# Kernel tuning notes

Hardware: AMD Instinct MI355X
Metric: run time of the kernel (lower is better)

## Reference

```python
import jax, jax.numpy as jnp
import numpy as np
from jax import lax

B, C_IN, C_OUT, K, N_W, L = 32, 256, 256, 7, 8, 4096
SQ = C_IN // 32  # squeezed dim = 8
STRIDE, PAD = 1, 3


def setup_inputs() -> dict:
    key = jax.random.key(0)
    ks = jax.random.split(key, 8)
    s = 0.05
    return {
        "x": jax.random.normal(ks[0], (B, C_IN, L), dtype=jnp.float32),
        "conv_weight": jax.random.normal(ks[1], (C_OUT, C_IN, K, N_W), dtype=jnp.float32) * s,
        "w1": jax.random.normal(ks[2], (C_IN, SQ), dtype=jnp.float32) * s,   # linear1 weight (x @ w1)
        "b1": jax.random.normal(ks[3], (SQ,), dtype=jnp.float32) * s,
        "wk": jax.random.normal(ks[4], (SQ, K), dtype=jnp.float32) * s,      # kernel head
        "wi": jax.random.normal(ks[5], (SQ, C_IN), dtype=jnp.float32) * s,   # inc head
        "wo": jax.random.normal(ks[6], (SQ, C_OUT), dtype=jnp.float32) * s,  # outc head
        "wn": jax.random.normal(ks[7], (SQ, N_W), dtype=jnp.float32) * s,    # nums head
    }


def reference(x, conv_weight, w1, b1, wk, wi, wo, wn):
    # SqueezeFeedForward: AdaptiveAvgPool1d(1) == mean over length, then Linear + exact GELU
    pooled = jnp.mean(x, axis=-1)                        # [B, C_in]
    h = jax.nn.gelu(pooled @ w1 + b1, approximate=False)  # [B, SQ]

    kr = jax.nn.sigmoid(h @ wk)          # [B, K]
    inc = jax.nn.sigmoid(h @ wi)         # [B, C_in]
    outc = jax.nn.sigmoid(h @ wo)        # [B, C_out]
    nums = jax.nn.softmax(h @ wn, -1)    # [B, N_w]

    # Per-sample mixed weights: sum over num_weight of 4-way outer-product gated base weight
    w = jnp.einsum('bk,bi,bo,bn,oikn->boik', kr, inc, outc, nums, conv_weight)  # [B,O,I,K]

    b, o, i, k = w.shape
    l = x.shape[-1]
    # Batched per-sample conv via grouped conv: groups = B
    lhs = x.reshape(1, b * i, l)         # [1, B*I, L]
    rhs = w.reshape(b * o, i, k)         # [B*O, I, K]
    out = lax.conv_general_dilated(
        lhs, rhs,
        window_strides=(STRIDE,),
        padding=[(PAD, PAD)],
        dimension_numbers=('NCH', 'OIH', 'NCH'),
        feature_group_count=b,
    )
    return out.reshape(b, o, -1)         # [B, O, L_out]
```

## Files before the change

### kernel.cpp

```cpp
#include <hip/hip_runtime.h>
#include <hip/hip_bf16.h>
#include <math.h>

#define B_   32
#define CI   256
#define CO   256
#define KW   7
#define NW   8
#define SQD  8
#define L_   4096

typedef __attribute__((ext_vector_type(8))) __bf16 bf16x8;
typedef __attribute__((ext_vector_type(4))) float  f32x4;

static __device__ __forceinline__ unsigned short f2bf(float f) {
    unsigned int u = __builtin_bit_cast(unsigned int, f);
    u += 0x7FFFu + ((u >> 16) & 1u);
    return (unsigned short)(u >> 16);
}

__global__ __launch_bounds__(256) void k1_mean(
        const float* __restrict__ x, float* __restrict__ pooled) {
    int row = blockIdx.x;
    const float* p = x + (size_t)row * L_;
    int t = threadIdx.x;
    float s = 0.f;
#pragma unroll
    for (int it = 0; it < 4; ++it) {
        float4 v = *(const float4*)(p + (size_t)(t + 256 * it) * 4);
        s += v.x + v.y + v.z + v.w;
    }
    for (int m = 1; m <= 32; m <<= 1) s += __shfl_xor(s, m);
    __shared__ float wsum[4];
    if ((t & 63) == 0) wsum[t >> 6] = s;
    __syncthreads();
    if (t == 0)
        pooled[row] = (wsum[0] + wsum[1] + wsum[2] + wsum[3]) * (1.0f / L_);
}

__global__ __launch_bounds__(64) void k2_gates(
        const float* __restrict__ pooled,
        const float* __restrict__ w1, const float* __restrict__ b1,
        const float* __restrict__ wk, const float* __restrict__ wi,
        const float* __restrict__ wo, const float* __restrict__ wn,
        float* __restrict__ kr,
        float* __restrict__ inc,
        float* __restrict__ outc,
        float* __restrict__ nums)
{
    int b = blockIdx.x, lane = threadIdx.x;
    float pc[4];
#pragma unroll
    for (int j = 0; j < 4; ++j)
        pc[j] = pooled[b * CI + lane + 64 * j];
    float h[SQD];
#pragma unroll
    for (int s = 0; s < SQD; ++s) {
        float ps = 0.f;
#pragma unroll
        for (int j = 0; j < 4; ++j)
            ps += pc[j] * w1[(lane + 64 * j) * SQD + s];
        for (int m = 1; m <= 32; m <<= 1) ps += __shfl_xor(ps, m);
        float z = ps + b1[s];
        h[s] = 0.5f * z * (1.0f + erff(z * 0.70710678118654752f));
    }
    if (lane < KW) {
        float a = 0.f;
#pragma unroll
        for (int s = 0; s < SQD; ++s) a += h[s] * wk[s * KW + lane];
        kr[b * 8 + lane] = 1.0f / (1.0f + expf(-a));
    }
    if (lane < NW) {
        float e[NW]; float mx = -1e30f;
#pragma unroll
        for (int n = 0; n < NW; ++n) {
            float a = 0.f;
#pragma unroll
            for (int s = 0; s < SQD; ++s) a += h[s] * wn[s * NW + n];
            e[n] = a; mx = fmaxf(mx, a);
        }
        float den = 0.f;
#pragma unroll
        for (int n = 0; n < NW; ++n) den += expf(e[n] - mx);
        nums[b * NW + lane] = expf(e[lane] - mx) / den;
    }
#pragma unroll
    for (int j = 0; j < 4; ++j) {
        int c = lane + 64 * j;
        float a = 0.f, o2 = 0.f;
#pragma unroll
        for (int s = 0; s < SQD; ++s) {
            a  += h[s] * wi[s * CI + c];
            o2 += h[s] * wo[s * CO + c];
        }
        inc[b * CI + c]  = 1.0f / (1.0f + expf(-a));
        outc[b * CO + c] = 1.0f / (1.0f + expf(-o2));
    }
}

__global__ __launch_bounds__(256) void k3_wgen(
        const float* __restrict__ cw,
        const float* __restrict__ kr, const float* __restrict__ inc,
        const float* __restrict__ outc, const float* __restrict__ nums,
        unsigned short* __restrict__ W2) {
    __shared__ float s_nums[B_][NW];
    __shared__ float s_kr[B_][KW];
    __shared__ float s_inc[B_][32];
    __shared__ float s_outc[B_][8];
    int t = threadIdx.x;
    int ic = blockIdx.x & 7, o0 = (blockIdx.x >> 3) * 8;
    s_nums[t >> 3][t & 7] = nums[t];
    if (t < B_ * KW) s_kr[t / KW][t % KW] = kr[(t / KW) * 8 + (t % KW)];
    for (int u = t; u < 32 * 32; u += 256) {
        int bb = u >> 5, ii = u & 31;
        s_inc[bb][ii] = inc[bb * CI + ic * 32 + ii];
    }
    for (int u = t; u < 32 * 8; u += 256) {
        int bb = u >> 3, oo = u & 7;
        s_outc[bb][oo] = outc[bb * CO + o0 + oo];
    }
    __syncthreads();
    int ii = t & 31, oo = t >> 5;
    int o = o0 + oo, i = ic * 32 + ii;
    float cwv[KW][NW];
    const float* p = cw + ((size_t)(o * CI + i)) * (KW * NW);
#pragma unroll
    for (int k = 0; k < KW; ++k)
#pragma unroll
        for (int n = 0; n < NW; ++n) cwv[k][n] = p[k * NW + n];
    for (int bb = 0; bb < B_; ++bb) {
        float gio = s_inc[bb][ii] * s_outc[bb][oo];
#pragma unroll
        for (int k = 0; k < KW; ++k) {
            float sk = 0.f;
#pragma unroll
            for (int n = 0; n < NW; ++n) sk += s_nums[bb][n] * cwv[k][n];
            float w = s_kr[bb][k] * gio * sk;
            W2[(((size_t)(bb * KW + k) * 8 + ic) * CO + o) * 32 + ii] = f2bf(w);
        }
    }
}

__global__ __launch_bounds__(512, 4) void k4_conv(
        const float* __restrict__ x,
        const unsigned short* __restrict__ W2,
        float* __restrict__ out) {
    __shared__ __align__(16) unsigned short xs[134 * 256];
    int bid = blockIdx.x;
    int wg  = (bid & 7) * 128 + (bid >> 3);
    int b = wg >> 5, l0 = (wg & 31) * 128;
    int t = threadIdx.x;
    const float* xb = x + (size_t)b * CI * L_;

    {
        int c = t & 31;
        int i = t >> 5;
#pragma unroll 4
        for (int it = 0; it < 16; ++it, i += 16) {
            float4 v = *(const float4*)(xb + (size_t)i * L_ + l0 + c * 4);
            int u0 = i >> 3, isub = i & 7;
#pragma unroll
            for (int j = 0; j < 4; ++j) {
                int r = c * 4 + j + 3;
                xs[r * 256 + ((u0 ^ (r & 7)) * 8) + isub] = f2bf((&v.x)[j]);
            }
        }
    }
    for (int u = t; u < 6 * 256; u += 512) {
        int h = u >> 8, i = u & 255;
        int r = (h < 3) ? h : 128 + h;
        int gl = l0 - 3 + r;
        float f = (gl >= 0 && gl < L_) ? xb[(size_t)i * L_ + gl] : 0.f;
        xs[r * 256 + (((i >> 3) ^ (r & 7)) * 8) + (i & 7)] = f2bf(f);
    }
    __syncthreads();

    int lane = t & 63, wid = t >> 6;
    int o_base = wid * 32;
    int ml = lane & 15, kg = lane >> 4;

    f32x4 acc[2][8];
#pragma unroll
    for (int a = 0; a < 2; ++a)
#pragma unroll
        for (int c = 0; c < 8; ++c) acc[a][c] = (f32x4){0.f, 0.f, 0.f, 0.f};

    const unsigned short* wbase = W2 + (size_t)b * (KW * 8 * CO * 32);
    for (int k = 0; k < KW; ++k) {
        const unsigned short* wk_ = wbase + (size_t)k * (8 * CO * 32);
#pragma unroll
        for (int icc = 0; icc < 8; ++icc) {
            const unsigned short* wkc = wk_ + icc * (CO * 32);
            bf16x8 af[2];
#pragma unroll
            for (int mt = 0; mt < 2; ++mt)
                af[mt] = *(const bf16x8*)(wkc + (o_base + mt * 16 + ml) * 32 + kg * 8);
            bf16x8 bfr[8];
#pragma unroll
            for (int nt = 0; nt < 8; ++nt) {
                int r = nt * 16 + ml + k;
                int unit = (icc * 4 + kg) ^ (r & 7);
                bfr[nt] = *(const bf16x8*)(xs + r * 256 + unit * 8);
            }
            __builtin_amdgcn_s_setprio(1);
#pragma unroll
            for (int mt = 0; mt < 2; ++mt)
#pragma unroll
                for (int nt = 0; nt < 8; ++nt)
                    acc[mt][nt] = __builtin_amdgcn_mfma_f32_16x16x32_bf16(
                        af[mt], bfr[nt], acc[mt][nt], 0, 0, 0);
            __builtin_amdgcn_s_setprio(0);
        }
    }

#pragma unroll
    for (int mt = 0; mt < 2; ++mt) {
        int o = o_base + mt * 16 + kg * 4;
#pragma unroll
        for (int nt = 0; nt < 8; ++nt) {
            int l = l0 + nt * 16 + ml;
            float* po = out + ((size_t)(b * CO + o)) * L_ + l;
#pragma unroll
            for (int q = 0; q < 4; ++q)
                po[(size_t)q * L_] = acc[mt][nt][q];
        }
    }
}

extern "C" void kernel_launch(void* const* d_in, const int* in_sizes, int n_in,
                              void* d_out, int out_size, void* d_ws, size_t ws_size,
                              hipStream_t stream) {
    const float* x  = (const float*)d_in[0];
    const float* cw = (const float*)d_in[1];
    const float* w1 = (const float*)d_in[2];
    const float* b1 = (const float*)d_in[3];
    const float* wk = (const float*)d_in[4];
    const float* wi = (const float*)d_in[5];
    const float* wo = (const float*)d_in[6];
    const float* wn = (const float*)d_in[7];
    float* out = (float*)d_out;

    char* ws = (char*)d_ws;
    const size_t off_W2     = 0;
    const size_t off_pooled = 29360128;
    const size_t off_kr     = 29392896;
    const size_t off_inc    = 29393920;
    const size_t off_outc   = 29426688;
    const size_t off_nums   = 29459456;

    unsigned short* W2 = (unsigned short*)(ws + off_W2);
    float* pooled = (float*)(ws + off_pooled);
    float* kr     = (float*)(ws + off_kr);
    float* inc    = (float*)(ws + off_inc);
    float* outc   = (float*)(ws + off_outc);
    float* nums   = (float*)(ws + off_nums);

    k1_mean<<<B_ * CI, 256, 0, stream>>>(x, pooled);
    k2_gates<<<B_, 64, 0, stream>>>(pooled, w1, b1, wk, wi, wo, wn,
                                    kr, inc, outc, nums);
    k3_wgen<<<256, 256, 0, stream>>>(cw, kr, inc, outc, nums, W2);
    k4_conv<<<1024, 512, 0, stream>>>(x, W2, out);
}
```

Measured before the change: 175.4 us.

## Enlarge conv tile to 256 positions, 2D warp split, and double-buffer fragments

The conv kernel now processes 256 length positions per block instead of 128, with 8 waves split as 4 output-channel groups × 2 length halves, each wave computing a 64x128 output tile (4x8 MFMA tiles). The wider tile doubles reuse of the weight fragments loaded from global memory and of the staged input. The input staging packs four channels per 8-byte LDS store and uses a new XOR swizzle. The main loop software-pipelines fragment loads with two register buffers so loads for the next step overlap the current MFMAs. The cost is more registers and twice the LDS (occupancy hint lowered to 2) and half as many blocks.

```diff
diff --git a/kernel.cpp b/kernel.cpp
--- a/kernel.cpp
+++ b/kernel.cpp
@@ -18,6 +18,9 @@
     u += 0x7FFFu + ((u >> 16) & 1u);
     return (unsigned short)(u >> 16);
 }
+static __device__ __forceinline__ unsigned int pack2bf(float a, float b) {
+    return (unsigned int)f2bf(a) | ((unsigned int)f2bf(b) << 16);
+}
 
 __global__ __launch_bounds__(256) void k1_mean(
         const float* __restrict__ x, float* __restrict__ pooled) {
@@ -43,10 +46,8 @@
         const float* __restrict__ w1, const float* __restrict__ b1,
         const float* __restrict__ wk, const float* __restrict__ wi,
         const float* __restrict__ wo, const float* __restrict__ wn,
-        float* __restrict__ kr,
-        float* __restrict__ inc,
-        float* __restrict__ outc,
-        float* __restrict__ nums)
+        float* __restrict__ kr, float* __restrict__ inc,
+        float* __restrict__ outc, float* __restrict__ nums)
 {
     int b = blockIdx.x, lane = threadIdx.x;
     float pc[4];
@@ -141,84 +142,117 @@
     }
 }
 
-__global__ __launch_bounds__(512, 4) void k4_conv(
+__global__ __launch_bounds__(512, 2) void k4_conv(
         const float* __restrict__ x,
         const unsigned short* __restrict__ W2,
         float* __restrict__ out) {
-    __shared__ __align__(16) unsigned short xs[134 * 256];
+    __shared__ __align__(16) unsigned short xs[262 * 256];
     int bid = blockIdx.x;
-    int wg  = (bid & 7) * 128 + (bid >> 3);
-    int b = wg >> 5, l0 = (wg & 31) * 128;
+    int wg  = (bid & 7) * 64 + (bid >> 3);
+    int b = wg >> 4, l0 = (wg & 15) * 256;
     int t = threadIdx.x;
     const float* xb = x + (size_t)b * CI * L_;
 
     {
-        int c = t & 31;
-        int i = t >> 5;
-#pragma unroll 4
-        for (int it = 0; it < 16; ++it, i += 16) {
-            float4 v = *(const float4*)(xb + (size_t)i * L_ + l0 + c * 4);
-            int u0 = i >> 3, isub = i & 7;
+        int ch = (t & 31) + 32 * (t >> 8);
+        int g  = (t >> 5) & 7;
+#pragma unroll
+        for (int it = 0; it < 8; ++it) {
+            int i0 = g * 4 + it * 32;
+            float4 f0 = *(const float4*)(xb + (size_t)(i0 + 0) * L_ + l0 + ch * 4);
+            float4 f1 = *(const float4*)(xb + (size_t)(i0 + 1) * L_ + l0 + ch * 4);
+            float4 f2 = *(const float4*)(xb + (size_t)(i0 + 2) * L_ + l0 + ch * 4);
+            float4 f3 = *(const float4*)(xb + (size_t)(i0 + 3) * L_ + l0 + ch * 4);
+            int u = i0 >> 3, h = (i0 >> 2) & 1;
 #pragma unroll
             for (int j = 0; j < 4; ++j) {
-                int r = c * 4 + j + 3;
-                xs[r * 256 + ((u0 ^ (r & 7)) * 8) + isub] = f2bf((&v.x)[j]);
+                int r = 4 * ch + j + 3;
+                uint2 w;
+                w.x = pack2bf((&f0.x)[j], (&f1.x)[j]);
+                w.y = pack2bf((&f2.x)[j], (&f3.x)[j]);
+                int sw = (r & 7) ^ ((r >> 2) & 7);
+                *(uint2*)(xs + r * 256 + ((u ^ sw) * 8) + h * 4) = w;
             }
         }
     }
-    for (int u = t; u < 6 * 256; u += 512) {
-        int h = u >> 8, i = u & 255;
-        int r = (h < 3) ? h : 128 + h;
-        int gl = l0 - 3 + r;
-        float f = (gl >= 0 && gl < L_) ? xb[(size_t)i * L_ + gl] : 0.f;
-        xs[r * 256 + (((i >> 3) ^ (r & 7)) * 8) + (i & 7)] = f2bf(f);
+    if (t < 128) {
+        bool left = t < 64;
+        int tt = left ? t : t - 64;
+        int i0 = tt * 4;
+        int gl4 = left ? l0 - 4 : l0 + 256;
+        bool ok = left ? (l0 > 0) : (l0 + 256 < L_);
+        float4 f[4];
+#pragma unroll
+        for (int d = 0; d < 4; ++d)
+            f[d] = ok ? *(const float4*)(xb + (size_t)(i0 + d) * L_ + gl4)
+                      : make_float4(0.f, 0.f, 0.f, 0.f);
+        int u = i0 >> 3, h = (i0 >> 2) & 1;
+#pragma unroll
+        for (int j = 0; j < 4; ++j) {
+            if (left && j == 0) continue;
+            if (!left && j == 3) continue;
+            int r = left ? (j - 1) : (259 + j);
+            uint2 w;
+            w.x = pack2bf((&f[0].x)[j], (&f[1].x)[j]);
+            w.y = pack2bf((&f[2].x)[j], (&f[3].x)[j]);
+            int sw = (r & 7) ^ ((r >> 2) & 7);
+            *(uint2*)(xs + r * 256 + ((u ^ sw) * 8) + h * 4) = w;
+        }
     }
     __syncthreads();
 
     int lane = t & 63, wid = t >> 6;
-    int o_base = wid * 32;
+    int o_base = (wid & 3) * 64;
+    int l_off  = (wid >> 2) * 128;
     int ml = lane & 15, kg = lane >> 4;
 
-    f32x4 acc[2][8];
-#pragma unroll
-    for (int a = 0; a < 2; ++a)
+    f32x4 acc[4][8];
+#pragma unroll
+    for (int a = 0; a < 4; ++a)
 #pragma unroll
         for (int c = 0; c < 8; ++c) acc[a][c] = (f32x4){0.f, 0.f, 0.f, 0.f};
 
-    const unsigned short* wbase = W2 + (size_t)b * (KW * 8 * CO * 32);
-    for (int k = 0; k < KW; ++k) {
-        const unsigned short* wk_ = wbase + (size_t)k * (8 * CO * 32);
-#pragma unroll
-        for (int icc = 0; icc < 8; ++icc) {
-            const unsigned short* wkc = wk_ + icc * (CO * 32);
-            bf16x8 af[2];
-#pragma unroll
-            for (int mt = 0; mt < 2; ++mt)
-                af[mt] = *(const bf16x8*)(wkc + (o_base + mt * 16 + ml) * 32 + kg * 8);
-            bf16x8 bfr[8];
-#pragma unroll
-            for (int nt = 0; nt < 8; ++nt) {
-                int r = nt * 16 + ml + k;
-                int unit = (icc * 4 + kg) ^ (r & 7);
-                bfr[nt] = *(const bf16x8*)(xs + r * 256 + unit * 8);
-            }
-            __builtin_amdgcn_s_setprio(1);
-#pragma unroll
-            for (int mt = 0; mt < 2; ++mt)
-#pragma unroll
-                for (int nt = 0; nt < 8; ++nt)
-                    acc[mt][nt] = __builtin_amdgcn_mfma_f32_16x16x32_bf16(
-                        af[mt], bfr[nt], acc[mt][nt], 0, 0, 0);
-            __builtin_amdgcn_s_setprio(0);
-        }
-    }
-
-#pragma unroll
-    for (int mt = 0; mt < 2; ++mt) {
+    const unsigned short* wbase = W2 + (size_t)b * (56 * CO * 32);
+
+    auto LOADF = [&](bf16x8 (&AF)[4], bf16x8 (&BF)[8], int S) {
+        int k_ = S >> 3, icc_ = S & 7;
+        const unsigned short* wkc = wbase + (size_t)S * (CO * 32);
+#pragma unroll
+        for (int mt = 0; mt < 4; ++mt)
+            AF[mt] = *(const bf16x8*)(wkc + (o_base + mt * 16 + ml) * 32 + kg * 8);
+#pragma unroll
+        for (int nt = 0; nt < 8; ++nt) {
+            int r = l_off + nt * 16 + ml + k_;
+            int unit = (icc_ * 4 + kg) ^ ((r & 7) ^ ((r >> 2) & 7));
+            BF[nt] = *(const bf16x8*)(xs + r * 256 + unit * 8);
+        }
+    };
+    auto DOMFMA = [&](bf16x8 (&AF)[4], bf16x8 (&BF)[8]) {
+        __builtin_amdgcn_s_setprio(1);
+#pragma unroll
+        for (int mt = 0; mt < 4; ++mt)
+#pragma unroll
+            for (int nt = 0; nt < 8; ++nt)
+                acc[mt][nt] = __builtin_amdgcn_mfma_f32_16x16x32_bf16(
+                    AF[mt], BF[nt], acc[mt][nt], 0, 0, 0);
+        __builtin_amdgcn_s_setprio(0);
+    };
+
+    bf16x8 afA[4], bfA[8], afB[4], bfB[8];
+    LOADF(afA, bfA, 0);
+    for (int s = 0; s < 56; s += 2) {
+        LOADF(afB, bfB, s + 1);
+        DOMFMA(afA, bfA);
+        if (s + 2 < 56) LOADF(afA, bfA, s + 2);
+        DOMFMA(afB, bfB);
+    }
+
+#pragma unroll
+    for (int mt = 0; mt < 4; ++mt) {
         int o = o_base + mt * 16 + kg * 4;
 #pragma unroll
         for (int nt = 0; nt < 8; ++nt) {
-            int l = l0 + nt * 16 + ml;
+            int l = l0 + l_off + nt * 16 + ml;
             float* po = out + ((size_t)(b * CO + o)) * L_ + l;
 #pragma unroll
             for (int q = 0; q < 4; ++q)
@@ -241,23 +275,16 @@
     float* out = (float*)d_out;
 
     char* ws = (char*)d_ws;
-    const size_t off_W2     = 0;
-    const size_t off_pooled = 29360128;
-    const size_t off_kr     = 29392896;
-    const size_t off_inc    = 29393920;
-    const size_t off_outc   = 29426688;
-    const size_t off_nums   = 29459456;
-
-    unsigned short* W2 = (unsigned short*)(ws + off_W2);
-    float* pooled = (float*)(ws + off_pooled);
-    float* kr     = (float*)(ws + off_kr);
-    float* inc    = (float*)(ws + off_inc);
-    float* outc   = (float*)(ws + off_outc);
-    float* nums   = (float*)(ws + off_nums);
+    unsigned short* W2 = (unsigned short*)(ws + 0);
+    float* pooled = (float*)(ws + 29360128);
+    float* kr     = (float*)(ws + 29392896);
+    float* inc    = (float*)(ws + 29393920);
+    float* outc   = (float*)(ws + 29426688);
+    float* nums   = (float*)(ws + 29459456);
 
     k1_mean<<<B_ * CI, 256, 0, stream>>>(x, pooled);
     k2_gates<<<B_, 64, 0, stream>>>(pooled, w1, b1, wk, wi, wo, wn,
                                     kr, inc, outc, nums);
     k3_wgen<<<256, 256, 0, stream>>>(cw, kr, inc, outc, nums, W2);
-    k4_conv<<<1024, 512, 0, stream>>>(x, W2, out);
-}
+    k4_conv<<<512, 512, 0, stream>>>(x, W2, out);
+}
```

Measured after the change: 172.8 us. Within noise of the previous version (-1.5%).
